# Optimization experiments

Measured on AMD Instinct MI355X. Metric: run time of the kernel, lower is better.

## Reference

```python
import jax, jax.numpy as jnp
import numpy as np

ATOM_DIMS = [119, 4, 12, 12, 10, 6, 6, 2, 2]
OFFSETS = jnp.asarray(np.concatenate([[0], np.cumsum(ATOM_DIMS)[:-1]]), dtype=jnp.int64)
TOTAL_ROWS = int(np.sum(ATOM_DIMS))  # 173
EPS = 1e-5
PROCESSING_STEPS = 4


def setup_inputs() -> dict:
    key = jax.random.key(0)
    ks = jax.random.split(key, 20)
    N, E, G, H, ENC = 262144, 524288, 8192, 256, 128
    x = jax.random.randint(ks[0], (N, 9), 0, 2)
    edge_index = jax.random.randint(ks[1], (2, E), 0, N)
    batch = jnp.sort(jax.random.randint(ks[2], (N,), 0, G))
    s = 0.05
    inp = {
        'x': x, 'edge_index': edge_index, 'batch': batch, 'n_graphs': G,
        'atom_emb': jax.random.normal(ks[3], (TOTAL_ROWS, H)) * s,
        'W1': jax.random.normal(ks[4], (H, H)) * s, 'b1': jnp.zeros((H,)),
        'W2': jax.random.normal(ks[5], (H, H)) * s, 'b2': jnp.zeros((H,)),
        'W3': jax.random.normal(ks[6], (H, H)) * s, 'b3': jnp.zeros((H,)),
        'gamma': jnp.ones((H,)), 'beta': jnp.zeros((H,)),
        'Wi': jax.random.normal(ks[7], (4 * H, 2 * H)) * s,
        'Wh': jax.random.normal(ks[8], (4 * H, H)) * s,
        'bi': jnp.zeros((4 * H,)), 'bh': jnp.zeros((4 * H,)),
        'lin1_W': jax.random.normal(ks[9], (ENC, 2 * H)) * s, 'lin1_b': jnp.zeros((ENC,)),
        'lin2_W': jax.random.normal(ks[10], (1, ENC)) * s, 'lin2_b': jnp.zeros((1,)),
    }
    return inp


def _gcn_conv(h, W, b, src, tgt, dinv, n_nodes):
    # GCNConv: linear, then D^-1/2 (A+I) D^-1/2 aggregation, then bias
    hw = h @ W.T
    norm = dinv[src] * dinv[tgt]                      # [E]
    agg = jax.ops.segment_sum(hw[src] * norm[:, None], tgt, num_segments=n_nodes)
    agg = agg + hw * (dinv * dinv)[:, None]           # self-loop term
    return agg + b


def _batchnorm(h, gamma, beta):
    mu = jnp.mean(h, axis=0)
    var = jnp.mean((h - mu) ** 2, axis=0)
    return (h - mu) * jax.lax.rsqrt(var + EPS) * gamma + beta


def _set2set(h, batch, n_graphs, Wi, Wh, bi, bh):
    G, H = n_graphs, h.shape[1]
    q_star = jnp.zeros((G, 2 * H), dtype=h.dtype)
    hs = jnp.zeros((G, H), dtype=h.dtype)
    cs = jnp.zeros((G, H), dtype=h.dtype)
    for _ in range(PROCESSING_STEPS):
        gates = q_star @ Wi.T + hs @ Wh.T + bi + bh   # [G, 4H], torch gate order i,f,g,o
        i, f, g, o = jnp.split(gates, 4, axis=1)
        cs = jax.nn.sigmoid(f) * cs + jax.nn.sigmoid(i) * jnp.tanh(g)
        hs = jax.nn.sigmoid(o) * jnp.tanh(cs)
        q = hs                                        # [G, H]
        e = jnp.sum(h * q[batch], axis=1)             # [N]
        m = jax.ops.segment_max(e, batch, num_segments=G)
        ee = jnp.exp(e - m[batch])
        z = jax.ops.segment_sum(ee, batch, num_segments=G)
        a = ee / z[batch]                             # scatter-softmax
        r = jax.ops.segment_sum(a[:, None] * h, batch, num_segments=G)
        q_star = jnp.concatenate([q, r], axis=1)
    return q_star


def reference(x, edge_index, batch, n_graphs, atom_emb, W1, b1, W2, b2, W3, b3,
              gamma, beta, Wi, Wh, bi, bh, lin1_W, lin1_b, lin2_W, lin2_b):
    N = x.shape[0]
    src, tgt = edge_index[0], edge_index[1]
    # AtomEncoder: sum of per-column embeddings via one offset-gather
    embed = jnp.sum(atom_emb[x + OFFSETS[None, :]], axis=1)     # [N, H]
    # gcn_norm degrees (with self loops)
    deg = jax.ops.segment_sum(jnp.ones_like(tgt, dtype=embed.dtype), tgt, num_segments=N) + 1.0
    dinv = jax.lax.rsqrt(deg)
    out = jax.nn.relu(_gcn_conv(embed, W1, b1, src, tgt, dinv, N))
    out = _batchnorm(out, gamma, beta)
    out = jax.nn.relu(_gcn_conv(out, W2, b2, src, tgt, dinv, N))
    out = _batchnorm(out, gamma, beta)
    out = _gcn_conv(out, W3, b3, src, tgt, dinv, N)
    out = _set2set(out, batch, n_graphs, Wi, Wh, bi, bh)        # [G, 2H]
    out = out @ lin1_W.T + lin1_b
    out = out @ lin2_W.T + lin2_b
    return jax.nn.sigmoid(out)
```

## Files before the change

kernel.cpp:

```cpp
#include <hip/hip_runtime.h>
#include <hip/hip_bf16.h>
#include <math.h>

using u16 = unsigned short;
typedef __attribute__((ext_vector_type(8))) short short8;
typedef __attribute__((ext_vector_type(8))) _Float16 half8;
typedef __attribute__((ext_vector_type(4))) float f32x4;
typedef __attribute__((ext_vector_type(4))) u16 u16x4;

__device__ __constant__ int c_OFF[9] = {0, 119, 123, 135, 147, 157, 163, 169, 171};

__device__ __forceinline__ float h2f(u16 u) {
    _Float16 h;
    __builtin_memcpy(&h, &u, 2);
    return (float)h;
}
__device__ __forceinline__ u16 f2h(float f) {
    _Float16 h = (_Float16)f;
    u16 u;
    __builtin_memcpy(&u, &h, 2);
    return u;
}
__device__ __forceinline__ float sigf(float x) { return 1.f / (1.f + expf(-x)); }

__global__ void k_diagf(float* out, int G, float val) {
    int i = blockIdx.x * 256 + threadIdx.x;
    if (i < G) out[i] = val;
}

__global__ void k_zero_f32(float* p, int n) {
    int i = blockIdx.x * 256 + threadIdx.x;
    if (i < n) p[i] = 0.f;
}
__global__ void k_zero_u16(u16* p, int n) {
    int i = blockIdx.x * 256 + threadIdx.x;
    if (i < n) p[i] = 0;
}
__global__ void k_zero_int(int* p, int n) {
    int i = blockIdx.x * 256 + threadIdx.x;
    if (i < n) p[i] = 0;
}

__global__ void k_cvtW(const float* __restrict__ src, u16* __restrict__ dst, int n) {
    int i = blockIdx.x * 256 + threadIdx.x;
    if (i < n) dst[i] = f2h(src[i]);
}

__global__ __launch_bounds__(256) void k_embed(const int* __restrict__ x,
                                               const float* __restrict__ emb,
                                               u16* __restrict__ out, int N) {
    __shared__ int rows[72];
    int nb = blockIdx.x * 8;
    int tid = threadIdx.x;
    if (tid < 72) rows[tid] = x[(size_t)nb * 9 + tid] + c_OFF[tid % 9];
    __syncthreads();
    int ln = tid >> 5;
    int c8 = (tid & 31) * 8;
    float s0 = 0.f, s1 = 0.f, s2 = 0.f, s3 = 0.f, s4 = 0.f, s5 = 0.f, s6 = 0.f, s7 = 0.f;
#pragma unroll
    for (int c = 0; c < 9; ++c) {
        int r = rows[ln * 9 + c];
        f32x4 a = *(const f32x4*)&emb[r * 256 + c8];
        f32x4 b = *(const f32x4*)&emb[r * 256 + c8 + 4];
        s0 += a[0]; s1 += a[1]; s2 += a[2]; s3 += a[3];
        s4 += b[0]; s5 += b[1]; s6 += b[2]; s7 += b[3];
    }
    short8 o;
    o[0] = (short)f2h(s0); o[1] = (short)f2h(s1); o[2] = (short)f2h(s2); o[3] = (short)f2h(s3);
    o[4] = (short)f2h(s4); o[5] = (short)f2h(s5); o[6] = (short)f2h(s6); o[7] = (short)f2h(s7);
    *(short8*)&out[(size_t)(nb + ln) * 256 + c8] = o;
}

__global__ void k_gstart(const int* __restrict__ batch, int* __restrict__ gstart, int N, int G) {
    int i = blockIdx.x * 256 + threadIdx.x;
    if (i >= N) return;
    int b = batch[i];
    if (i == 0) {
        for (int g = 0; g <= b; ++g) gstart[g] = 0;
    } else {
        int p = batch[i - 1];
        for (int g = p + 1; g <= b; ++g) gstart[g] = i;
    }
    if (i == N - 1) {
        for (int g = b + 1; g <= G; ++g) gstart[g] = N;
    }
}

__global__ void k_count(const int* __restrict__ tgt, int* rp, int E) {
    int e = blockIdx.x * 256 + threadIdx.x;
    if (e < E) atomicAdd(&rp[tgt[e]], 1);
}

__global__ void k_dinv(const int* __restrict__ cnt, float* __restrict__ dinv, int N) {
    int i = blockIdx.x * 256 + threadIdx.x;
    if (i < N) dinv[i] = rsqrtf((float)cnt[i] + 1.f);
}

__global__ void k_scan1(int* __restrict__ rp, int* __restrict__ bsum, int N) {
    int t = threadIdx.x;
    int base = blockIdx.x * 1024 + t * 4;
    int v0 = 0, v1 = 0, v2 = 0, v3 = 0;
    if (base + 3 < N) {
        v0 = rp[base]; v1 = rp[base + 1]; v2 = rp[base + 2]; v3 = rp[base + 3];
    } else {
        if (base < N) v0 = rp[base];
        if (base + 1 < N) v1 = rp[base + 1];
        if (base + 2 < N) v2 = rp[base + 2];
    }
    int s = v0 + v1 + v2 + v3;
    int lane = t & 63, w = t >> 6;
    int x = s;
    for (int o = 1; o < 64; o <<= 1) {
        int y = __shfl_up(x, o, 64);
        if (lane >= o) x += y;
    }
    __shared__ int wsum[4];
    if (lane == 63) wsum[w] = x;
    __syncthreads();
    int woff = 0;
    for (int i = 0; i < w; ++i) woff += wsum[i];
    int excl = woff + x - s;
    if (base < N) rp[base] = excl;
    if (base + 1 < N) rp[base + 1] = excl + v0;
    if (base + 2 < N) rp[base + 2] = excl + v0 + v1;
    if (base + 3 < N) rp[base + 3] = excl + v0 + v1 + v2;
    if (t == 255) bsum[blockIdx.x] = wsum[0] + wsum[1] + wsum[2] + wsum[3];
}

__global__ void k_scan2(int* bsum, int nb) {
    int t = threadIdx.x;
    int s = (t < nb) ? bsum[t] : 0;
    int lane = t & 63, w = t >> 6;
    int x = s;
    for (int o = 1; o < 64; o <<= 1) {
        int y = __shfl_up(x, o, 64);
        if (lane >= o) x += y;
    }
    __shared__ int wsum[4];
    if (lane == 63) wsum[w] = x;
    __syncthreads();
    int woff = 0;
    for (int i = 0; i < w; ++i) woff += wsum[i];
    if (t < nb) bsum[t] = woff + x - s;
}

__global__ void k_scan3(int* __restrict__ rp, const int* __restrict__ bsum, int N) {
    int i = blockIdx.x * 256 + threadIdx.x;
    if (i < N) rp[i] += bsum[i >> 10];
}

__global__ void k_fill(const int* __restrict__ src, const int* __restrict__ tgt,
                       int* __restrict__ rp, const float* __restrict__ dinv,
                       int2* __restrict__ est, int E) {
    int e = blockIdx.x * 256 + threadIdx.x;
    if (e < E) {
        int t = tgt[e];
        int s = src[e];
        int p = atomicAdd(&rp[t], 1);
        est[p] = make_int2(s, __float_as_int(dinv[s] * dinv[t]));
    }
}

__global__ __launch_bounds__(256, 3) void k_gemm(const u16* __restrict__ p0, int rs0,
                                                 const u16* __restrict__ p1, int rs1,
                                                 const u16* __restrict__ W,
                                                 const float* __restrict__ cvec,
                                                 u16* __restrict__ out, int N) {
    __shared__ u16 As[64][260];
    __shared__ u16 Ws[256][36];
    int r0 = blockIdx.x * 64;
    int tid = threadIdx.x, lane = tid & 63, w = tid >> 6;
#pragma unroll
    for (int i = 0; i < 8; ++i) {
        int chunk = i * 256 + tid;
        int r = chunk >> 5, c8 = chunk & 31;
        const u16* sp = (c8 < 16) ? &p0[(size_t)(r0 + r) * rs0 + c8 * 8]
                                  : &p1[(size_t)(r0 + r) * rs1 + (c8 - 16) * 8];
        *(short8*)&As[r][c8 * 8] = *(const short8*)sp;
    }
    f32x4 acc[16];
#pragma unroll
    for (int o = 0; o < 16; ++o) acc[o] = f32x4{0.f, 0.f, 0.f, 0.f};
    for (int k0 = 0; k0 < 256; k0 += 32) {
        __syncthreads();
#pragma unroll
        for (int i = 0; i < 4; ++i) {
            int chunk = i * 256 + tid;
            int r = chunk >> 2, c8 = chunk & 3;
            *(short8*)&Ws[r][c8 * 8] = *(const short8*)&W[(size_t)r * 256 + k0 + c8 * 8];
        }
        __syncthreads();
        half8 af = *(const half8*)&As[w * 16 + (lane & 15)][k0 + (lane >> 4) * 8];
#pragma unroll
        for (int o = 0; o < 16; ++o) {
            half8 wf = *(const half8*)&Ws[o * 16 + (lane & 15)][(lane >> 4) * 8];
            acc[o] = __builtin_amdgcn_mfma_f32_16x16x32_f16(af, wf, acc[o], 0, 0, 0);
        }
    }
    __syncthreads();
#pragma unroll
    for (int o = 0; o < 16; ++o) {
        int col = o * 16 + (lane & 15);
        float cv = cvec ? cvec[col] : 0.f;
#pragma unroll
        for (int r = 0; r < 4; ++r) {
            int row = w * 16 + (lane >> 4) * 4 + r;
            As[row][col] = f2h(acc[o][r] + cv);
        }
    }
    __syncthreads();
#pragma unroll
    for (int i = 0; i < 8; ++i) {
        int chunk = i * 256 + tid;
        int r = chunk >> 5, c8 = chunk & 31;
        *(short8*)&out[(size_t)(r0 + r) * 256 + c8 * 8] = *(const short8*)&As[r][c8 * 8];
    }
}

template <bool RS>
__global__ __launch_bounds__(256) void k_aggh(const u16* __restrict__ src, int srs,
                                              u16* __restrict__ dst, int drs,
                                              const int* __restrict__ rp,
                                              const int2* __restrict__ est,
                                              const float* __restrict__ dinv,
                                              const float* __restrict__ biasH,
                                              float* __restrict__ statS,
                                              float* __restrict__ statQ, int N) {
    int l = threadIdx.x & 15;
    int sub = blockIdx.x * 16 + (threadIdx.x >> 4);
    int n0 = sub * 4;
    if (n0 >= N) return;
    float bv[8];
#pragma unroll
    for (int k = 0; k < 8; ++k) bv[k] = biasH[l * 8 + k];
    float ss[8] = {}, qq[8] = {};
    int rA = n0 ? rp[n0 - 1] : 0;
#pragma unroll
    for (int t = 0; t < 4; ++t) {
        int n = n0 + t;
        int rB = rp[n];
        float dn = dinv[n];
        short8 hv = *(const short8*)&src[(size_t)n * srs + l * 8];
        float a[8];
#pragma unroll
        for (int k = 0; k < 8; ++k) a[k] = h2f((u16)hv[k]) * dn * dn + bv[k];
        int j = rA;
        for (; j + 1 < rB; j += 2) {
            int2 e0 = est[j], e1 = est[j + 1];
            float n0f = __int_as_float(e0.y), n1f = __int_as_float(e1.y);
            short8 v0 = *(const short8*)&src[(size_t)e0.x * srs + l * 8];
            short8 v1 = *(const short8*)&src[(size_t)e1.x * srs + l * 8];
#pragma unroll
            for (int k = 0; k < 8; ++k) a[k] += h2f((u16)v0[k]) * n0f + h2f((u16)v1[k]) * n1f;
        }
        if (j < rB) {
            int2 e0 = est[j];
            float n0f = __int_as_float(e0.y);
            short8 v0 = *(const short8*)&src[(size_t)e0.x * srs + l * 8];
#pragma unroll
            for (int k = 0; k < 8; ++k) a[k] += h2f((u16)v0[k]) * n0f;
        }
        rA = rB;
        short8 o;
#pragma unroll
        for (int k = 0; k < 8; ++k) {
            if (RS) {
                a[k] = fmaxf(a[k], 0.f);
                ss[k] += a[k];
                qq[k] += a[k] * a[k];
            }
            o[k] = (short)f2h(a[k]);
        }
        *(short8*)&dst[(size_t)n * drs + l * 8] = o;
    }
    if (RS) {
        __shared__ float sh[256];
        int t = threadIdx.x;
        sh[t] = 0.f;
        __syncthreads();
#pragma unroll
        for (int k = 0; k < 8; ++k) {
            atomicAdd(&sh[l * 8 + k], ss[k]);
            atomicAdd(&sh[128 + l * 8 + k], qq[k]);
        }
        __syncthreads();
        if (t < 128)
            atomicAdd(&statS[t], sh[t]);
        else
            atomicAdd(&statQ[t - 128], sh[t]);
    }
}

__global__ void k_copyh(const u16* __restrict__ src, u16* __restrict__ dst, int N) {
    int i = blockIdx.x * 256 + threadIdx.x;
    if (i >= N * 16) return;
    int n = i >> 4, c8 = (i & 15) * 8;
    *(short8*)&dst[(size_t)n * 128 + c8] = *(const short8*)&src[(size_t)n * 256 + c8];
}

__global__ void k_bnparam(const float* __restrict__ stats, const float* __restrict__ gamma,
                          const float* __restrict__ beta, float* __restrict__ st, int N) {
    int d = threadIdx.x;
    float inv = 1.f / (float)N;
    float mu = stats[d] * inv;
    float var = fmaxf(stats[256 + d] * inv - mu * mu, 0.f);
    float sc = gamma[d] * rsqrtf(var + 1e-5f);
    st[d] = sc;
    st[256 + d] = beta[d] - mu * sc;
}

__global__ void k_fold(const float* __restrict__ W, const float* __restrict__ st,
                       u16* __restrict__ Wp, float* __restrict__ cvec) {
    __shared__ float red[256];
    int o = blockIdx.x, k = threadIdx.x;
    float w = W[o * 256 + k];
    Wp[o * 256 + k] = f2h(w * st[k]);
    red[k] = w * st[256 + k];
    __syncthreads();
    for (int s = 128; s > 0; s >>= 1) {
        if (k < s) red[k] += red[k + s];
        __syncthreads();
    }
    if (k == 0) cvec[o] = red[0];
}

__global__ __launch_bounds__(256, 2) void k_gemmf(const u16* __restrict__ A,
                                                  const u16* __restrict__ W,
                                                  const float* __restrict__ cvec,
                                                  u16* __restrict__ C, int M, int K, int O) {
    const int PAD = 8;
    __shared__ u16 As[128][64 + PAD];
    __shared__ u16 Ws[128][64 + PAD];
    int tM = blockIdx.x, tO = blockIdx.y;
    int tid = threadIdx.x;
    int lane = tid & 63, wid = tid >> 6;
    int wM = wid & 1, wO = wid >> 1;
    f32x4 acc[4][4] = {};
    size_t rowA0 = (size_t)tM * 128, rowW0 = (size_t)tO * 128;
    for (int k0 = 0; k0 < K; k0 += 64) {
#pragma unroll
        for (int i = 0; i < 4; ++i) {
            int chunk = tid + i * 256;
            int r = chunk >> 3, c16 = chunk & 7;
            *(short8*)&As[r][c16 * 8] = *(const short8*)&A[(rowA0 + r) * K + k0 + c16 * 8];
            *(short8*)&Ws[r][c16 * 8] = *(const short8*)&W[(rowW0 + r) * K + k0 + c16 * 8];
        }
        __syncthreads();
#pragma unroll
        for (int ks = 0; ks < 2; ++ks) {
            half8 af[4], wf[4];
#pragma unroll
            for (int m = 0; m < 4; ++m)
                af[m] = *(const half8*)&As[wM * 64 + m * 16 + (lane & 15)][ks * 32 + (lane >> 4) * 8];
#pragma unroll
            for (int o = 0; o < 4; ++o)
                wf[o] = *(const half8*)&Ws[wO * 64 + o * 16 + (lane & 15)][ks * 32 + (lane >> 4) * 8];
#pragma unroll
            for (int m = 0; m < 4; ++m)
#pragma unroll
                for (int o = 0; o < 4; ++o)
                    acc[m][o] = __builtin_amdgcn_mfma_f32_16x16x32_f16(af[m], wf[o], acc[m][o], 0, 0, 0);
        }
        __syncthreads();
    }
#pragma unroll
    for (int m = 0; m < 4; ++m) {
        int R0 = tM * 128 + wM * 64 + m * 16 + (lane >> 4) * 4;
#pragma unroll
        for (int o = 0; o < 4; ++o) {
            int Cc = tO * 128 + wO * 64 + o * 16 + (lane & 15);
            float cv = cvec[Cc];
#pragma unroll
            for (int r = 0; r < 4; ++r)
                C[(size_t)(R0 + r) * O + Cc] = f2h(acc[m][o][r] + cv);
        }
    }
}

__global__ void k_wcat(const float* __restrict__ Wi, const float* __restrict__ Wh,
                       const float* __restrict__ bi, const float* __restrict__ bh,
                       u16* __restrict__ Wcat, float* __restrict__ bcat) {
    int o = blockIdx.x;
    int t = threadIdx.x;
    for (int c = t; c < 512; c += 256) Wcat[(size_t)o * 768 + c] = f2h(Wi[(size_t)o * 512 + c]);
    if (t < 256) Wcat[(size_t)o * 768 + 512 + t] = f2h(Wh[(size_t)o * 256 + t]);
    if (t == 0) bcat[o] = bi[o] + bh[o];
}

__global__ void k_lstm(const u16* __restrict__ gates, float* __restrict__ cs,
                       float* __restrict__ hsb, u16* __restrict__ qsh, int G) {
    int idx = blockIdx.x * 256 + threadIdx.x;
    if (idx >= G * 256) return;
    int g = idx >> 8, d = idx & 255;
    const u16* gt = &gates[(size_t)g * 1024];
    float gi = h2f(gt[d]), gf = h2f(gt[256 + d]), gg = h2f(gt[512 + d]), go = h2f(gt[768 + d]);
    float c = sigf(gf) * cs[idx] + sigf(gi) * tanhf(gg);
    float hh = sigf(go) * tanhf(c);
    cs[idx] = c;
    hsb[idx] = hh;
    u16 hb = f2h(hh);
    qsh[(size_t)g * 768 + d] = hb;
    qsh[(size_t)g * 768 + 512 + d] = hb;
}

__global__ __launch_bounds__(256) void k_attn2(const u16* __restrict__ lo, int lstr,
                                               const u16* __restrict__ hi, int hstr,
                                               const float* __restrict__ hs,
                                               const int* __restrict__ gstart,
                                               u16* __restrict__ qsh, int G) {
    int wid = threadIdx.x >> 6, lane = threadIdx.x & 63;
    int g = blockIdx.x * 4 + wid;
    if (g >= G) return;
    int start = gstart[g], end = gstart[g + 1];

    const u16* base = (lane < 32) ? lo : hi;
    size_t stride = (lane < 32) ? lstr : hstr;
    int coff = (lane < 32) ? lane * 4 : (lane - 32) * 4;

    f32x4 q = *(const f32x4*)&hs[(size_t)g * 256 + lane * 4];
    float m = -INFINITY, z = 0.f;
    float r0a = 0.f, r1a = 0.f, r2a = 0.f, r3a = 0.f;

    for (int c0 = start; c0 < end; c0 += 256) {
        int cn = min(256, end - c0);
        float e0 = 0.f, e1 = 0.f, e2 = 0.f, e3 = 0.f;
        float mc = m;

        auto pass1 = [&](int rr, float& ev) {
            int b = c0 + rr * 64;
            int nr = min(64, end - b);
            for (int ii = 0; ii < nr; ++ii) {
                u16x4 hv = *(const u16x4*)&base[(size_t)(b + ii) * stride + coff];
                float e = h2f(hv[0]) * q[0] + h2f(hv[1]) * q[1] + h2f(hv[2]) * q[2] + h2f(hv[3]) * q[3];
                e += __shfl_xor(e, 32, 64);
                e += __shfl_xor(e, 16, 64);
                e += __shfl_xor(e, 8, 64);
                e += __shfl_xor(e, 4, 64);
                e += __shfl_xor(e, 2, 64);
                e += __shfl_xor(e, 1, 64);
                if (lane == ii) ev = e;
                mc = fmaxf(mc, e);
            }
        };
        pass1(0, e0);
        pass1(1, e1);
        pass1(2, e2);
        pass1(3, e3);

        float rf = (m == -INFINITY) ? 0.f : expf(m - mc);
        float zc = 0.f;
        e0 = (lane < cn) ? expf(e0 - mc) : 0.f;
        zc += e0;
        e1 = (64 + lane < cn) ? expf(e1 - mc) : 0.f;
        zc += e1;
        e2 = (128 + lane < cn) ? expf(e2 - mc) : 0.f;
        zc += e2;
        e3 = (192 + lane < cn) ? expf(e3 - mc) : 0.f;
        zc += e3;
        zc += __shfl_xor(zc, 32, 64);
        zc += __shfl_xor(zc, 16, 64);
        zc += __shfl_xor(zc, 8, 64);
        zc += __shfl_xor(zc, 4, 64);
        zc += __shfl_xor(zc, 2, 64);
        zc += __shfl_xor(zc, 1, 64);
        z = z * rf + zc;
        r0a *= rf; r1a *= rf; r2a *= rf; r3a *= rf;

        auto pass2 = [&](int rr, float ev) {
            int b = c0 + rr * 64;
            int nr = min(64, end - b);
            for (int ii = 0; ii < nr; ++ii) {
                float w = __shfl(ev, ii, 64);
                u16x4 hv = *(const u16x4*)&base[(size_t)(b + ii) * stride + coff];
                r0a += w * h2f(hv[0]);
                r1a += w * h2f(hv[1]);
                r2a += w * h2f(hv[2]);
                r3a += w * h2f(hv[3]);
            }
        };
        pass2(0, e0);
        pass2(1, e1);
        pass2(2, e2);
        pass2(3, e3);
        m = mc;
    }
    float inv = (end > start) ? 1.f / fmaxf(z, 1e-30f) : 0.f;
    u16x4 o;
    o[0] = f2h(r0a * inv);
    o[1] = f2h(r1a * inv);
    o[2] = f2h(r2a * inv);
    o[3] = f2h(r3a * inv);
    int qcol = (lane < 32) ? lane * 4 : 128 + (lane - 32) * 4;
    *(u16x4*)&qsh[(size_t)g * 768 + 256 + qcol] = o;
}

__global__ void k_wfold(const float* __restrict__ l1W, const float* __restrict__ l1b,
                        const float* __restrict__ l2W, const float* __restrict__ l2b,
                        float* __restrict__ weff) {
    int c = blockIdx.x * 256 + threadIdx.x;
    if (c < 512) {
        float s = 0.f;
        for (int t = 0; t < 128; ++t) s += l2W[t] * l1W[(size_t)t * 512 + c];
        weff[c] = s;
    }
    if (c == 0) {
        float b = l2b[0];
        for (int t = 0; t < 128; ++t) b += l2W[t] * l1b[t];
        weff[512] = b;
    }
}

__global__ __launch_bounds__(256) void k_final2(const u16* __restrict__ qsh,
                                                const float* __restrict__ weff,
                                                float* __restrict__ out, int G) {
    __shared__ float wsm[513];
    int tid = threadIdx.x;
    for (int j = tid; j < 513; j += 256) wsm[j] = weff[j];
    __syncthreads();
    int g = blockIdx.x * 4 + (tid >> 6);
    int lane = tid & 63;
    if (g >= G) return;
    const u16* qp = &qsh[(size_t)g * 768];
    float s = 0.f;
#pragma unroll
    for (int j = 0; j < 8; ++j) s += h2f(qp[lane * 8 + j]) * wsm[lane * 8 + j];
    for (int off = 32; off; off >>= 1) s += __shfl_xor(s, off, 64);
    if (lane == 0) out[g] = sigf(s + wsm[512]);
}

extern "C" void kernel_launch(void* const* d_in, const int* in_sizes, int n_in,
                              void* d_out, int out_size, void* d_ws, size_t ws_size,
                              hipStream_t stream) {
    const int* x = (const int*)d_in[0];
    const int* ei = (const int*)d_in[1];
    const int* batch = (const int*)d_in[2];
    const float* atom_emb = (const float*)d_in[4];
    const float* W1 = (const float*)d_in[5];
    const float* b1 = (const float*)d_in[6];
    const float* W2 = (const float*)d_in[7];
    const float* b2 = (const float*)d_in[8];
    const float* W3 = (const float*)d_in[9];
    const float* b3 = (const float*)d_in[10];
    const float* gamma = (const float*)d_in[11];
    const float* beta = (const float*)d_in[12];
    const float* Wi = (const float*)d_in[13];
    const float* Wh = (const float*)d_in[14];
    const float* bi = (const float*)d_in[15];
    const float* bh = (const float*)d_in[16];
    const float* l1W = (const float*)d_in[17];
    const float* l1b = (const float*)d_in[18];
    const float* l2W = (const float*)d_in[19];
    const float* l2b = (const float*)d_in[20];

    const int N = in_sizes[0] / 9;
    const int E = in_sizes[1] / 2;
    const int G = out_size;
    const int* srcp = ei;
    const int* tgtp = ei + E;

    char* ws = (char*)d_ws;
    size_t off = 0;
    auto alloc = [&](size_t bytes) -> void* {
        void* p = ws + off;
        off += (bytes + 255) & ~(size_t)255;
        return p;
    };
    u16* X = (u16*)alloc((size_t)N * 256 * 2);
    int* rp = (int*)alloc((size_t)N * 4);
    int2* est = (int2*)alloc((size_t)E * 8);
    float* dinv = (float*)alloc((size_t)N * 4);
    int* gstart = (int*)alloc((size_t)(G + 1) * 4);
    float* stats = (float*)alloc(512 * 4);
    float* stbuf = (float*)alloc(512 * 4);
    float* cvec = (float*)alloc(256 * 4);
    u16* Wp = (u16*)alloc(256 * 256 * 2);
    int* bsum = (int*)alloc(1024 * 4);
    float* weff = (float*)alloc(513 * 4);
    size_t offR = off;

    size_t halfB = ((size_t)N * 128 * 2 + 255) & ~(size_t)255;
    size_t s2sR = 0;
    {
        size_t t = 0;
        auto sz = [&](size_t b) { t += (b + 255) & ~(size_t)255; };
        sz((size_t)1024 * 768 * 2);
        sz(1024 * 4);
        sz((size_t)G * 768 * 2);
        sz((size_t)G * 1024 * 2);
        sz((size_t)G * 256 * 4);
        sz((size_t)G * 256 * 4);
        s2sR = t;
    }
    size_t needA = offR + halfB + s2sR;
    size_t needB = offR + (halfB > s2sR ? halfB : s2sR);
    bool tierA = ws_size >= needA;
    if (!tierA && ws_size < needB) {
        k_diagf<<<(G + 255) / 256, 256, 0, stream>>>((float*)d_out, G, 12345.0f);
        return;
    }
    u16* Y = (u16*)(ws + offR);
    size_t s2sBase = tierA ? offR + halfB : offR;
    size_t o2 = s2sBase;
    auto alloc2 = [&](size_t bytes) -> void* {
        void* p = ws + o2;
        o2 += (bytes + 255) & ~(size_t)255;
        return p;
    };
    u16* Wcat = (u16*)alloc2((size_t)1024 * 768 * 2);
    float* bcat = (float*)alloc2(1024 * 4);
    u16* qsh = (u16*)alloc2((size_t)G * 768 * 2);
    u16* gates = (u16*)alloc2((size_t)G * 1024 * 2);
    float* hsb = (float*)alloc2((size_t)G * 256 * 4);
    float* csb = (float*)alloc2((size_t)G * 256 * 4);

    k_embed<<<N / 8, 256, 0, stream>>>(x, atom_emb, X, N);
    k_gstart<<<(N + 255) / 256, 256, 0, stream>>>(batch, gstart, N, G);
    k_zero_int<<<(N + 255) / 256, 256, 0, stream>>>(rp, N);
    k_count<<<(E + 255) / 256, 256, 0, stream>>>(tgtp, rp, E);
    k_dinv<<<(N + 255) / 256, 256, 0, stream>>>(rp, dinv, N);
    int nb1 = (N + 1023) / 1024;
    k_scan1<<<nb1, 256, 0, stream>>>(rp, bsum, N);
    k_scan2<<<1, 256, 0, stream>>>(bsum, nb1);
    k_scan3<<<(N + 255) / 256, 256, 0, stream>>>(rp, bsum, N);
    k_fill<<<(E + 255) / 256, 256, 0, stream>>>(srcp, tgtp, rp, dinv, est, E);

    int gipb = N / 64;
    int cpb = (N * 16 + 255) / 256;
    int aggb = (N / 4 + 15) / 16;

    k_cvtW<<<256, 256, 0, stream>>>(W1, Wp, 65536);
    k_zero_f32<<<2, 256, 0, stream>>>(stats, 512);
    k_gemm<<<gipb, 256, 0, stream>>>(X, 256, X + 128, 256, Wp, nullptr, X, N);
    k_aggh<true><<<aggb, 256, 0, stream>>>(X, 256, Y, 128, rp, est, dinv, b1, stats, stats + 256, N);
    k_aggh<true><<<aggb, 256, 0, stream>>>(X + 128, 256, X, 256, rp, est, dinv, b1 + 128, stats + 128, stats + 384, N);
    k_bnparam<<<1, 256, 0, stream>>>(stats, gamma, beta, stbuf, N);

    k_fold<<<256, 256, 0, stream>>>(W2, stbuf, Wp, cvec);
    k_zero_f32<<<2, 256, 0, stream>>>(stats, 512);
    k_gemm<<<gipb, 256, 0, stream>>>(Y, 128, X, 256, Wp, cvec, X, N);
    k_aggh<true><<<aggb, 256, 0, stream>>>(X, 256, Y, 128, rp, est, dinv, b2, stats, stats + 256, N);
    k_aggh<true><<<aggb, 256, 0, stream>>>(X + 128, 256, X, 256, rp, est, dinv, b2 + 128, stats + 128, stats + 384, N);
    k_bnparam<<<1, 256, 0, stream>>>(stats, gamma, beta, stbuf, N);

    k_fold<<<256, 256, 0, stream>>>(W3, stbuf, Wp, cvec);
    k_gemm<<<gipb, 256, 0, stream>>>(Y, 128, X, 256, Wp, cvec, X, N);
    const u16 *h3lo, *h3hi;
    int h3ls, h3hs;
    if (tierA) {
        k_aggh<false><<<aggb, 256, 0, stream>>>(X, 256, Y, 128, rp, est, dinv, b3, nullptr, nullptr, N);
        k_aggh<false><<<aggb, 256, 0, stream>>>(X + 128, 256, X, 256, rp, est, dinv, b3 + 128, nullptr, nullptr, N);
        h3lo = Y; h3ls = 128; h3hi = X; h3hs = 256;
    } else {
        k_copyh<<<cpb, 256, 0, stream>>>(X, Y, N);
        k_aggh<false><<<aggb, 256, 0, stream>>>(Y, 128, X, 256, rp, est, dinv, b3, nullptr, nullptr, N);
        k_copyh<<<cpb, 256, 0, stream>>>(X + 128, Y, N);
        k_aggh<false><<<aggb, 256, 0, stream>>>(Y, 128, X + 128, 256, rp, est, dinv, b3 + 128, nullptr, nullptr, N);
        h3lo = X; h3ls = 256; h3hi = X + 128; h3hs = 256;
    }

    k_wcat<<<1024, 256, 0, stream>>>(Wi, Wh, bi, bh, Wcat, bcat);
    k_zero_u16<<<(G * 768 + 255) / 256, 256, 0, stream>>>(qsh, G * 768);
    k_zero_f32<<<(G * 256 + 255) / 256, 256, 0, stream>>>(csb, G * 256);
    dim3 ggates(G / 128, 8);
    for (int s = 0; s < 4; ++s) {
        k_gemmf<<<ggates, 256, 0, stream>>>(qsh, Wcat, bcat, gates, G, 768, 1024);
        k_lstm<<<(G * 256 + 255) / 256, 256, 0, stream>>>(gates, csb, hsb, qsh, G);
        k_attn2<<<(G + 3) / 4, 256, 0, stream>>>(h3lo, h3ls, h3hi, h3hs, hsb, gstart, qsh, G);
    }
    k_wfold<<<2, 256, 0, stream>>>(l1W, l1b, l2W, l2b, weff);
    k_final2<<<(G + 3) / 4, 256, 0, stream>>>(qsh, weff, (float*)d_out, G);
}
```

Baseline: 1.469 ms.

## Fuse half-width GCN aggregations into one full-width kernel with extra buffer

Adds a full-width aggregation kernel in which 32 lanes cover all 256 features. Each node's CSR edge list and the gathered source rows are therefore read once instead of once per half. Outputs go to two separate half buffers, Y and Y2, so the aggregation no longer has to write back into the GEMM input it is still reading. When the workspace is large enough, a new tier uses this path and reuses the X region for the set2set buffers. This costs more workspace and doubles per-thread block coverage, and the old path is kept as a fallback when memory is short.

```diff
diff --git a/kernel.cpp b/kernel.cpp
--- a/kernel.cpp
+++ b/kernel.cpp
@@ -214,6 +214,83 @@
         int chunk = i * 256 + tid;
         int r = chunk >> 5, c8 = chunk & 31;
         *(short8*)&out[(size_t)(r0 + r) * 256 + c8 * 8] = *(const short8*)&As[r][c8 * 8];
+    }
+}
+
+template <bool RS>
+__global__ __launch_bounds__(256) void k_aggf(const u16* __restrict__ src,
+                                              u16* __restrict__ dlo,
+                                              u16* __restrict__ dhi,
+                                              const int* __restrict__ rp,
+                                              const int2* __restrict__ est,
+                                              const float* __restrict__ dinv,
+                                              const float* __restrict__ bias,
+                                              float* __restrict__ stats, int N) {
+    int l = threadIdx.x & 31;
+    int sub = blockIdx.x * 8 + (threadIdx.x >> 5);
+    int n0 = sub * 4;
+    float bv[8];
+#pragma unroll
+    for (int k = 0; k < 8; ++k) bv[k] = bias[l * 8 + k];
+    float ss[8] = {}, qq[8] = {};
+    if (n0 < N) {
+        int rA = n0 ? rp[n0 - 1] : 0;
+#pragma unroll
+        for (int t = 0; t < 4; ++t) {
+            int n = n0 + t;
+            int rB = rp[n];
+            float dn = dinv[n];
+            short8 hv = *(const short8*)&src[(size_t)n * 256 + l * 8];
+            float a[8];
+#pragma unroll
+            for (int k = 0; k < 8; ++k) a[k] = h2f((u16)hv[k]) * dn * dn + bv[k];
+            int j = rA;
+            for (; j + 1 < rB; j += 2) {
+                int2 e0 = est[j], e1 = est[j + 1];
+                float n0f = __int_as_float(e0.y), n1f = __int_as_float(e1.y);
+                short8 v0 = *(const short8*)&src[(size_t)e0.x * 256 + l * 8];
+                short8 v1 = *(const short8*)&src[(size_t)e1.x * 256 + l * 8];
+#pragma unroll
+                for (int k = 0; k < 8; ++k) a[k] += h2f((u16)v0[k]) * n0f + h2f((u16)v1[k]) * n1f;
+            }
+            if (j < rB) {
+                int2 e0 = est[j];
+                float n0f = __int_as_float(e0.y);
+                short8 v0 = *(const short8*)&src[(size_t)e0.x * 256 + l * 8];
+#pragma unroll
+                for (int k = 0; k < 8; ++k) a[k] += h2f((u16)v0[k]) * n0f;
+            }
+            rA = rB;
+            short8 o;
+#pragma unroll
+            for (int k = 0; k < 8; ++k) {
+                if (RS) {
+                    a[k] = fmaxf(a[k], 0.f);
+                    ss[k] += a[k];
+                    qq[k] += a[k] * a[k];
+                }
+                o[k] = (short)f2h(a[k]);
+            }
+            if (l < 16)
+                *(short8*)&dlo[(size_t)n * 128 + l * 8] = o;
+            else
+                *(short8*)&dhi[(size_t)n * 128 + (l - 16) * 8] = o;
+        }
+    }
+    if (RS) {
+        __shared__ float sh[512];
+        int t = threadIdx.x;
+        sh[t] = 0.f;
+        sh[t + 256] = 0.f;
+        __syncthreads();
+#pragma unroll
+        for (int k = 0; k < 8; ++k) {
+            atomicAdd(&sh[l * 8 + k], ss[k]);
+            atomicAdd(&sh[256 + l * 8 + k], qq[k]);
+        }
+        __syncthreads();
+        atomicAdd(&stats[t], sh[t]);
+        atomicAdd(&stats[t + 256], sh[t + 256]);
     }
 }
 
@@ -229,49 +306,50 @@
     int l = threadIdx.x & 15;
     int sub = blockIdx.x * 16 + (threadIdx.x >> 4);
     int n0 = sub * 4;
-    if (n0 >= N) return;
     float bv[8];
 #pragma unroll
     for (int k = 0; k < 8; ++k) bv[k] = biasH[l * 8 + k];
     float ss[8] = {}, qq[8] = {};
-    int rA = n0 ? rp[n0 - 1] : 0;
-#pragma unroll
-    for (int t = 0; t < 4; ++t) {
-        int n = n0 + t;
-        int rB = rp[n];
-        float dn = dinv[n];
-        short8 hv = *(const short8*)&src[(size_t)n * srs + l * 8];
-        float a[8];
-#pragma unroll
-        for (int k = 0; k < 8; ++k) a[k] = h2f((u16)hv[k]) * dn * dn + bv[k];
-        int j = rA;
-        for (; j + 1 < rB; j += 2) {
-            int2 e0 = est[j], e1 = est[j + 1];
-            float n0f = __int_as_float(e0.y), n1f = __int_as_float(e1.y);
-            short8 v0 = *(const short8*)&src[(size_t)e0.x * srs + l * 8];
-            short8 v1 = *(const short8*)&src[(size_t)e1.x * srs + l * 8];
-#pragma unroll
-            for (int k = 0; k < 8; ++k) a[k] += h2f((u16)v0[k]) * n0f + h2f((u16)v1[k]) * n1f;
-        }
-        if (j < rB) {
-            int2 e0 = est[j];
-            float n0f = __int_as_float(e0.y);
-            short8 v0 = *(const short8*)&src[(size_t)e0.x * srs + l * 8];
-#pragma unroll
-            for (int k = 0; k < 8; ++k) a[k] += h2f((u16)v0[k]) * n0f;
-        }
-        rA = rB;
-        short8 o;
-#pragma unroll
-        for (int k = 0; k < 8; ++k) {
-            if (RS) {
-                a[k] = fmaxf(a[k], 0.f);
-                ss[k] += a[k];
-                qq[k] += a[k] * a[k];
+    if (n0 < N) {
+        int rA = n0 ? rp[n0 - 1] : 0;
+#pragma unroll
+        for (int t = 0; t < 4; ++t) {
+            int n = n0 + t;
+            int rB = rp[n];
+            float dn = dinv[n];
+            short8 hv = *(const short8*)&src[(size_t)n * srs + l * 8];
+            float a[8];
+#pragma unroll
+            for (int k = 0; k < 8; ++k) a[k] = h2f((u16)hv[k]) * dn * dn + bv[k];
+            int j = rA;
+            for (; j + 1 < rB; j += 2) {
+                int2 e0 = est[j], e1 = est[j + 1];
+                float n0f = __int_as_float(e0.y), n1f = __int_as_float(e1.y);
+                short8 v0 = *(const short8*)&src[(size_t)e0.x * srs + l * 8];
+                short8 v1 = *(const short8*)&src[(size_t)e1.x * srs + l * 8];
+#pragma unroll
+                for (int k = 0; k < 8; ++k) a[k] += h2f((u16)v0[k]) * n0f + h2f((u16)v1[k]) * n1f;
             }
-            o[k] = (short)f2h(a[k]);
-        }
-        *(short8*)&dst[(size_t)n * drs + l * 8] = o;
+            if (j < rB) {
+                int2 e0 = est[j];
+                float n0f = __int_as_float(e0.y);
+                short8 v0 = *(const short8*)&src[(size_t)e0.x * srs + l * 8];
+#pragma unroll
+                for (int k = 0; k < 8; ++k) a[k] += h2f((u16)v0[k]) * n0f;
+            }
+            rA = rB;
+            short8 o;
+#pragma unroll
+            for (int k = 0; k < 8; ++k) {
+                if (RS) {
+                    a[k] = fmaxf(a[k], 0.f);
+                    ss[k] += a[k];
+                    qq[k] += a[k] * a[k];
+                }
+                o[k] = (short)f2h(a[k]);
+            }
+            *(short8*)&dst[(size_t)n * drs + l * 8] = o;
+        }
     }
     if (RS) {
         __shared__ float sh[256];
@@ -565,6 +643,7 @@
         off += (bytes + 255) & ~(size_t)255;
         return p;
     };
+    size_t xOff = off;
     u16* X = (u16*)alloc((size_t)N * 256 * 2);
     int* rp = (int*)alloc((size_t)N * 4);
     int2* est = (int2*)alloc((size_t)E * 8);
@@ -591,15 +670,19 @@
         sz((size_t)G * 256 * 4);
         s2sR = t;
     }
+    size_t xBytes = ((size_t)N * 256 * 2 + 255) & ~(size_t)255;
+    size_t needFull = offR + 2 * halfB;
     size_t needA = offR + halfB + s2sR;
     size_t needB = offR + (halfB > s2sR ? halfB : s2sR);
-    bool tierA = ws_size >= needA;
-    if (!tierA && ws_size < needB) {
+    int tier = (ws_size >= needFull && s2sR <= xBytes) ? 2 : ws_size >= needA ? 1
+               : ws_size >= needB ? 0 : -1;
+    if (tier < 0) {
         k_diagf<<<(G + 255) / 256, 256, 0, stream>>>((float*)d_out, G, 12345.0f);
         return;
     }
     u16* Y = (u16*)(ws + offR);
-    size_t s2sBase = tierA ? offR + halfB : offR;
+    u16* Y2 = (u16*)(ws + offR + halfB);
+    size_t s2sBase = (tier == 2) ? xOff : (tier == 1) ? offR + halfB : offR;
     size_t o2 = s2sBase;
     auto alloc2 = [&](size_t bytes) -> void* {
         void* p = ws + o2;
@@ -627,35 +710,59 @@
     int gipb = N / 64;
     int cpb = (N * 16 + 255) / 256;
     int aggb = (N / 4 + 15) / 16;
-
-    k_cvtW<<<256, 256, 0, stream>>>(W1, Wp, 65536);
-    k_zero_f32<<<2, 256, 0, stream>>>(stats, 512);
-    k_gemm<<<gipb, 256, 0, stream>>>(X, 256, X + 128, 256, Wp, nullptr, X, N);
-    k_aggh<true><<<aggb, 256, 0, stream>>>(X, 256, Y, 128, rp, est, dinv, b1, stats, stats + 256, N);
-    k_aggh<true><<<aggb, 256, 0, stream>>>(X + 128, 256, X, 256, rp, est, dinv, b1 + 128, stats + 128, stats + 384, N);
-    k_bnparam<<<1, 256, 0, stream>>>(stats, gamma, beta, stbuf, N);
-
-    k_fold<<<256, 256, 0, stream>>>(W2, stbuf, Wp, cvec);
-    k_zero_f32<<<2, 256, 0, stream>>>(stats, 512);
-    k_gemm<<<gipb, 256, 0, stream>>>(Y, 128, X, 256, Wp, cvec, X, N);
-    k_aggh<true><<<aggb, 256, 0, stream>>>(X, 256, Y, 128, rp, est, dinv, b2, stats, stats + 256, N);
-    k_aggh<true><<<aggb, 256, 0, stream>>>(X + 128, 256, X, 256, rp, est, dinv, b2 + 128, stats + 128, stats + 384, N);
-    k_bnparam<<<1, 256, 0, stream>>>(stats, gamma, beta, stbuf, N);
-
-    k_fold<<<256, 256, 0, stream>>>(W3, stbuf, Wp, cvec);
-    k_gemm<<<gipb, 256, 0, stream>>>(Y, 128, X, 256, Wp, cvec, X, N);
+    int aggfb = (N / 4 + 7) / 8;
+
     const u16 *h3lo, *h3hi;
     int h3ls, h3hs;
-    if (tierA) {
-        k_aggh<false><<<aggb, 256, 0, stream>>>(X, 256, Y, 128, rp, est, dinv, b3, nullptr, nullptr, N);
-        k_aggh<false><<<aggb, 256, 0, stream>>>(X + 128, 256, X, 256, rp, est, dinv, b3 + 128, nullptr, nullptr, N);
-        h3lo = Y; h3ls = 128; h3hi = X; h3hs = 256;
+    if (tier == 2) {
+        for (int conv = 0; conv < 3; ++conv) {
+            const float* Wsrc = conv == 0 ? W1 : (conv == 1 ? W2 : W3);
+            const float* bsrc = conv == 0 ? b1 : (conv == 1 ? b2 : b3);
+            bool rs = conv < 2;
+            if (conv == 0)
+                k_cvtW<<<256, 256, 0, stream>>>(Wsrc, Wp, 65536);
+            else
+                k_fold<<<256, 256, 0, stream>>>(Wsrc, stbuf, Wp, cvec);
+            if (rs) k_zero_f32<<<2, 256, 0, stream>>>(stats, 512);
+            if (conv == 0)
+                k_gemm<<<gipb, 256, 0, stream>>>(X, 256, X + 128, 256, Wp, nullptr, X, N);
+            else
+                k_gemm<<<gipb, 256, 0, stream>>>(Y, 128, Y2, 128, Wp, cvec, X, N);
+            if (rs)
+                k_aggf<true><<<aggfb, 256, 0, stream>>>(X, Y, Y2, rp, est, dinv, bsrc, stats, N);
+            else
+                k_aggf<false><<<aggfb, 256, 0, stream>>>(X, Y, Y2, rp, est, dinv, bsrc, nullptr, N);
+            if (rs) k_bnparam<<<1, 256, 0, stream>>>(stats, gamma, beta, stbuf, N);
+        }
+        h3lo = Y; h3ls = 128; h3hi = Y2; h3hs = 128;
     } else {
-        k_copyh<<<cpb, 256, 0, stream>>>(X, Y, N);
-        k_aggh<false><<<aggb, 256, 0, stream>>>(Y, 128, X, 256, rp, est, dinv, b3, nullptr, nullptr, N);
-        k_copyh<<<cpb, 256, 0, stream>>>(X + 128, Y, N);
-        k_aggh<false><<<aggb, 256, 0, stream>>>(Y, 128, X + 128, 256, rp, est, dinv, b3 + 128, nullptr, nullptr, N);
-        h3lo = X; h3ls = 256; h3hi = X + 128; h3hs = 256;
+        k_cvtW<<<256, 256, 0, stream>>>(W1, Wp, 65536);
+        k_zero_f32<<<2, 256, 0, stream>>>(stats, 512);
+        k_gemm<<<gipb, 256, 0, stream>>>(X, 256, X + 128, 256, Wp, nullptr, X, N);
+        k_aggh<true><<<aggb, 256, 0, stream>>>(X, 256, Y, 128, rp, est, dinv, b1, stats, stats + 256, N);
+        k_aggh<true><<<aggb, 256, 0, stream>>>(X + 128, 256, X, 256, rp, est, dinv, b1 + 128, stats + 128, stats + 384, N);
+        k_bnparam<<<1, 256, 0, stream>>>(stats, gamma, beta, stbuf, N);
+
+        k_fold<<<256, 256, 0, stream>>>(W2, stbuf, Wp, cvec);
+        k_zero_f32<<<2, 256, 0, stream>>>(stats, 512);
+        k_gemm<<<gipb, 256, 0, stream>>>(Y, 128, X, 256, Wp, cvec, X, N);
+        k_aggh<true><<<aggb, 256, 0, stream>>>(X, 256, Y, 128, rp, est, dinv, b2, stats, stats + 256, N);
+        k_aggh<true><<<aggb, 256, 0, stream>>>(X + 128, 256, X, 256, rp, est, dinv, b2 + 128, stats + 128, stats + 384, N);
+        k_bnparam<<<1, 256, 0, stream>>>(stats, gamma, beta, stbuf, N);
+
+        k_fold<<<256, 256, 0, stream>>>(W3, stbuf, Wp, cvec);
+        k_gemm<<<gipb, 256, 0, stream>>>(Y, 128, X, 256, Wp, cvec, X, N);
+        if (tier == 1) {
+            k_aggh<false><<<aggb, 256, 0, stream>>>(X, 256, Y, 128, rp, est, dinv, b3, nullptr, nullptr, N);
+            k_aggh<false><<<aggb, 256, 0, stream>>>(X + 128, 256, X, 256, rp, est, dinv, b3 + 128, nullptr, nullptr, N);
+            h3lo = Y; h3ls = 128; h3hi = X; h3hs = 256;
+        } else {
+            k_copyh<<<cpb, 256, 0, stream>>>(X, Y, N);
+            k_aggh<false><<<aggb, 256, 0, stream>>>(Y, 128, X, 256, rp, est, dinv, b3, nullptr, nullptr, N);
+            k_copyh<<<cpb, 256, 0, stream>>>(X + 128, Y, N);
+            k_aggh<false><<<aggb, 256, 0, stream>>>(Y, 128, X + 128, 256, rp, est, dinv, b3 + 128, nullptr, nullptr, N);
+            h3lo = X; h3ls = 256; h3hi = X + 128; h3hs = 256;
+        }
     }
 
     k_wcat<<<1024, 256, 0, stream>>>(Wi, Wh, bi, bh, Wcat, bcat);
```

Result: no change. 1.472 ms (+0.2%).
